# Kernel tuning notes

Hardware: AMD Instinct MI355X
Metric: run time of the kernel (lower is better)

The kernel has to match this reference:

```python
import jax, jax.numpy as jnp
import numpy as np

T = 1024
DIMS = 256


def setup_inputs() -> dict:
    key = jax.random.key(0)
    k1, k2, k3, k4 = jax.random.split(key, 4)
    k = jax.random.normal(k1, (T, DIMS), dtype=jnp.float32)
    v = jax.random.normal(k2, (T, DIMS), dtype=jnp.float32)
    time_first = jax.random.normal(k3, (DIMS,), dtype=jnp.float32)
    # time_decay must be negative so exp(decay * (i+1-j)) does not overflow
    # for lags up to T (torch.randn init would overflow at T=1024).
    time_decay = -(jax.random.uniform(k4, (DIMS,), dtype=jnp.float32) * 4.0 + 0.1)
    return {"k": k, "v": v, "time_first": time_first, "time_decay": time_decay}


def reference(k, v, time_first, time_decay):
    T_, D = k.shape
    idx = jnp.arange(T_)
    mask = idx[:, None] >= idx[None, :]                      # [T,T] causal (tril)
    # tri[i,j] = i+1-j on/below diagonal, 0 above (matches torch .tril())
    tri = jnp.where(mask, (idx[:, None] + 1 - idx[None, :]), 0).astype(k.dtype)
    # t[i,j,d] = exp(time_decay[d] * tri[i,j]) * mask[i,j]   # [T,T,D] ~1GB
    t = jnp.exp(time_decay[None, None, :] * tri[:, :, None]) * mask[:, :, None]
    kx = jnp.exp(k)                                          # [T,D]
    vx = v * kx                                              # [T,D]
    kxr = jnp.einsum('ijd,jd->id', t, kx)                    # decay-weighted causal sums
    vxr = jnp.einsum('ijd,jd->id', t, vx)
    tf = jnp.exp(time_first)                                 # [D]
    # Faithful to source: numerator uses kxr, denominator uses vxr (as written).
    vxx = vx * tf + kxr
    kxx = kx * tf + vxr
    return vxx / kxx
```

## Files before the change

### kernel.cpp

```cpp
#include <hip/hip_runtime.h>


constexpr int T = 1024;
constexpr int D = 256;
constexpr int L = 4;

__global__ __launch_bounds__(256) void wkv_scan_kernel(
    const float* __restrict__ k, const float* __restrict__ v,
    const float* __restrict__ time_first, const float* __restrict__ time_decay,
    float* __restrict__ out)
{
    const int d    = blockIdx.x;
    const int t    = threadIdx.x;
    const int lane = t & 63;
    const int wv   = t >> 6;

    const float td = time_decay[d];
    const float wd = __expf(td);
    const float tf = __expf(time_first[d]);

    const int base = t * L;

    float kx[L], vx[L];
    float bk = 0.f, bv = 0.f;
#pragma unroll
    for (int j = 0; j < L; ++j) {
        const float kk = k[(base + j) * D + d];
        const float vv = v[(base + j) * D + d];
        const float e  = __expf(kk);
        kx[j] = e;
        vx[j] = vv * e;
        bk = wd * (kx[j] + bk);
        bv = wd * (vx[j] + bv);
    }

    float f = __expf(td * (float)L);
#pragma unroll
    for (int o = 1; o < 64; o <<= 1) {
        const float pk = __shfl_up(bk, o);
        const float pv = __shfl_up(bv, o);
        if (lane >= o) {
            bk = fmaf(f, pk, bk);
            bv = fmaf(f, pv, bv);
        }
        f = f * f;
    }

    __shared__ float wbk[4], wbv[4];
    if (lane == 63) { wbk[wv] = bk; wbv[wv] = bv; }
    __syncthreads();
    const float m256 = __expf(td * (float)(L * 64));
    float Pk = 0.f, Pv = 0.f;
    for (int u = 0; u < wv; ++u) {
        Pk = fmaf(m256, Pk, wbk[u]);
        Pv = fmaf(m256, Pv, wbv[u]);
    }

    float ek = __shfl_up(bk, 1);
    float ev = __shfl_up(bv, 1);
    if (lane == 0) { ek = 0.f; ev = 0.f; }
    const float mlane = __expf(td * (float)(L * lane));
    float sk = fmaf(mlane, Pk, ek);
    float sv = fmaf(mlane, Pv, ev);

#pragma unroll
    for (int j = 0; j < L; ++j) {
        sk = wd * (kx[j] + sk);
        sv = wd * (vx[j] + sv);
        const float num = fmaf(vx[j], tf, sk);
        const float den = fmaf(kx[j], tf, sv);
        out[(base + j) * D + d] = num * __builtin_amdgcn_rcpf(den);
    }
}

extern "C" void kernel_launch(void* const* d_in, const int* in_sizes, int n_in,
                              void* d_out, int out_size, void* d_ws, size_t ws_size,
                              hipStream_t stream) {
    const float* k  = (const float*)d_in[0];
    const float* v  = (const float*)d_in[1];
    const float* tf = (const float*)d_in[2];
    const float* td = (const float*)d_in[3];
    float* out = (float*)d_out;

    dim3 grid(D);
    dim3 block(256);
    wkv_scan_kernel<<<grid, block, 0, stream>>>(k, v, tf, td, out);
}
```

Before: 11.83 us.

## Split scan into three kernels for coalesced carry, scan, and apply passes

Splits the single per-channel kernel into three launches. The first computes per-chunk carries with coalesced loads across channels, the second scans the carries per channel, and the third re-reads k and v coalesced to produce the output. The goal is to replace the old strided access, where each block read one column with a stride of D, with coalesced row access. The cost is two extra kernel launches, workspace round trips, and reading k and v twice.

```diff
diff --git a/kernel.cpp b/kernel.cpp
--- a/kernel.cpp
+++ b/kernel.cpp
@@ -4,11 +4,36 @@
 constexpr int T = 1024;
 constexpr int D = 256;
 constexpr int L = 4;
+constexpr int NC = T / L;
 
-__global__ __launch_bounds__(256) void wkv_scan_kernel(
+__global__ __launch_bounds__(256) void k1_carries(
     const float* __restrict__ k, const float* __restrict__ v,
-    const float* __restrict__ time_first, const float* __restrict__ time_decay,
-    float* __restrict__ out)
+    const float* __restrict__ time_decay,
+    float* __restrict__ bk_ws, float* __restrict__ bv_ws)
+{
+    const int c = blockIdx.x;
+    const int d = threadIdx.x;
+    const float td = time_decay[d];
+    const float wd = __expf(td);
+    const int base = c * L;
+
+    float bk = 0.f, bv = 0.f;
+#pragma unroll
+    for (int j = 0; j < L; ++j) {
+        const float kk = k[(base + j) * D + d];
+        const float vv = v[(base + j) * D + d];
+        const float e  = __expf(kk);
+        bk = wd * (e + bk);
+        bv = wd * (vv * e + bv);
+    }
+    bk_ws[c * D + d] = bk;
+    bv_ws[c * D + d] = bv;
+}
+
+__global__ __launch_bounds__(256) void k2_scan(
+    const float* __restrict__ time_decay,
+    const float* __restrict__ bk_ws, const float* __restrict__ bv_ws,
+    float* __restrict__ pk_ws, float* __restrict__ pv_ws)
 {
     const int d    = blockIdx.x;
     const int t    = threadIdx.x;
@@ -16,23 +41,8 @@
     const int wv   = t >> 6;
 
     const float td = time_decay[d];
-    const float wd = __expf(td);
-    const float tf = __expf(time_first[d]);
-
-    const int base = t * L;
-
-    float kx[L], vx[L];
-    float bk = 0.f, bv = 0.f;
-#pragma unroll
-    for (int j = 0; j < L; ++j) {
-        const float kk = k[(base + j) * D + d];
-        const float vv = v[(base + j) * D + d];
-        const float e  = __expf(kk);
-        kx[j] = e;
-        vx[j] = vv * e;
-        bk = wd * (kx[j] + bk);
-        bv = wd * (vx[j] + bv);
-    }
+    float bk = bk_ws[t * D + d];
+    float bv = bv_ws[t * D + d];
 
     float f = __expf(td * (float)L);
 #pragma unroll
@@ -60,15 +70,35 @@
     float ev = __shfl_up(bv, 1);
     if (lane == 0) { ek = 0.f; ev = 0.f; }
     const float mlane = __expf(td * (float)(L * lane));
-    float sk = fmaf(mlane, Pk, ek);
-    float sv = fmaf(mlane, Pv, ev);
+    pk_ws[t * D + d] = fmaf(mlane, Pk, ek);
+    pv_ws[t * D + d] = fmaf(mlane, Pv, ev);
+}
 
+__global__ __launch_bounds__(256) void k3_apply(
+    const float* __restrict__ k, const float* __restrict__ v,
+    const float* __restrict__ time_first, const float* __restrict__ time_decay,
+    const float* __restrict__ pk_ws, const float* __restrict__ pv_ws,
+    float* __restrict__ out)
+{
+    const int c = blockIdx.x;
+    const int d = threadIdx.x;
+    const float td = time_decay[d];
+    const float wd = __expf(td);
+    const float tf = __expf(time_first[d]);
+    const int base = c * L;
+
+    float sk = pk_ws[c * D + d];
+    float sv = pv_ws[c * D + d];
 #pragma unroll
     for (int j = 0; j < L; ++j) {
-        sk = wd * (kx[j] + sk);
-        sv = wd * (vx[j] + sv);
-        const float num = fmaf(vx[j], tf, sk);
-        const float den = fmaf(kx[j], tf, sv);
+        const float kk = k[(base + j) * D + d];
+        const float vv = v[(base + j) * D + d];
+        const float e  = __expf(kk);
+        const float vx = vv * e;
+        sk = wd * (e + sk);
+        sv = wd * (vx + sv);
+        const float num = fmaf(vx, tf, sk);
+        const float den = fmaf(e,  tf, sv);
         out[(base + j) * D + d] = num * __builtin_amdgcn_rcpf(den);
     }
 }
@@ -82,7 +112,13 @@
     const float* td = (const float*)d_in[3];
     float* out = (float*)d_out;
 
-    dim3 grid(D);
-    dim3 block(256);
-    wkv_scan_kernel<<<grid, block, 0, stream>>>(k, v, tf, td, out);
+    float* ws = (float*)d_ws;
+    float* bk_ws = ws;
+    float* bv_ws = ws + NC * D;
+    float* pk_ws = ws + 2 * NC * D;
+    float* pv_ws = ws + 3 * NC * D;
+
+    k1_carries<<<dim3(NC), dim3(D), 0, stream>>>(k, v, td, bk_ws, bv_ws);
+    k2_scan   <<<dim3(D), dim3(NC), 0, stream>>>(td, bk_ws, bv_ws, pk_ws, pv_ws);
+    k3_apply  <<<dim3(NC), dim3(D), 0, stream>>>(k, v, tf, td, pk_ws, pv_ws, out);
 }
```

Result: slower. 15.83 us (+33.8%).
